# Kernel tuning notes

Hardware: AMD Instinct MI355X
Metric: run time of the kernel (lower is better)

## Reference

```python
import jax, jax.numpy as jnp
import numpy as np

# static config (matches init_kwargs / input_specs)
LENS = (2048, 1024, 512, 256)   # per-level temporal lengths, sum = 3840
N, LQ, D_MODEL = 8, 2048, 256
M, L, P = 8, 4, 4               # heads, levels, points
D_HEAD = D_MODEL // M           # 32


def setup_inputs() -> dict:
    key = jax.random.key(0)
    ks = jax.random.split(key, 8)
    s = 0.02  # xavier-ish scale for 256-wide linears
    return {
        "query": jax.random.normal(ks[0], (N, LQ, D_MODEL), jnp.float32),
        "reference_points": jax.random.uniform(ks[1], (N, LQ, L, 1), dtype=jnp.float32),
        "input_flatten": jax.random.normal(ks[2], (N, sum(LENS), D_MODEL), jnp.float32),
        "input_temporal_lens": jnp.array(LENS, jnp.int32),
        "input_level_start_index": jnp.array(np.concatenate([[0], np.cumsum(LENS)[:-1]]), jnp.int32),
        "W_val": jax.random.normal(ks[3], (D_MODEL, D_MODEL), jnp.float32) * s,
        "b_val": jnp.zeros((D_MODEL,), jnp.float32),
        "W_off": jax.random.normal(ks[4], (M * L * P, D_MODEL), jnp.float32) * s,
        "b_off": jax.random.normal(ks[5], (M * L * P,), jnp.float32),  # mimics linspace bias init
        "W_attn": jax.random.normal(ks[6], (M * L * P, D_MODEL), jnp.float32) * s,
        "b_attn": jnp.zeros((M * L * P,), jnp.float32),
    }


def _sample_level(v, x, T):
    """1D bilinear sampling with zero padding, matching F.grid_sample
    (mode='bilinear', padding_mode='zeros', align_corners=False) on a (1,T) map.
    v: (N, T, M, D) level values; x: (N, Lq, M, P) normalized locations in [0,1].
    Returns (N, Lq, M, P, D)."""
    n, lq, m, p = x.shape
    ix = x * T - 0.5
    ix0 = jnp.floor(ix)
    w1 = (ix - ix0)[..., None]            # (N,Lq,M,P,1)
    i0 = ix0.astype(jnp.int32)

    def gather(idx):
        valid = ((idx >= 0) & (idx < T)).astype(v.dtype)
        idxc = jnp.clip(idx, 0, T - 1)
        flat = idxc.transpose(0, 1, 3, 2).reshape(n, lq * p, m)       # (N, Lq*P, M)
        g = jnp.take_along_axis(v, flat[..., None], axis=1)           # (N, Lq*P, M, D)
        g = g * valid.transpose(0, 1, 3, 2).reshape(n, lq * p, m)[..., None]
        return g.reshape(n, lq, p, m, -1).transpose(0, 1, 3, 2, 4)    # (N,Lq,M,P,D)

    return gather(i0) * (1.0 - w1) + gather(i0 + 1) * w1


def _deform_core(value, lens, loc, attn):
    """value: (N, S, M, D); loc: (N,Lq,M,L,P,1); attn: (N,Lq,M,L,P) -> (N,Lq,M*D)"""
    out = 0.0
    start = 0
    for lid, T in enumerate(lens):
        v = value[:, start:start + T]
        start += T
        s = _sample_level(v, loc[:, :, :, lid, :, 0], T)              # (N,Lq,M,P,D)
        out = out + jnp.einsum('nqmpd,nqmp->nqmd', s, attn[:, :, :, lid])
    n, lq, m, d = out.shape
    return out.reshape(n, lq, m * d)


def reference(query, reference_points, input_flatten, input_temporal_lens,
              input_level_start_index, W_val, b_val, W_off, b_off, W_attn, b_attn):
    lens = LENS  # static per-level lengths (needed for static slicing)
    value = (input_flatten @ W_val.T + b_val).reshape(N, sum(lens), M, D_HEAD)
    offs = (query @ W_off.T + b_off).reshape(N, LQ, M, L, P, 1)
    attn = jax.nn.softmax((query @ W_attn.T + b_attn).reshape(N, LQ, M, L * P), axis=-1)
    attn = attn.reshape(N, LQ, M, L, P)
    # reference_points last dim == 1, offset_normalizer=None branch
    norm = jnp.asarray(lens, query.dtype)[None, None, None, :, None, None]
    loc = reference_points[:, :, None, :, None, :] + offs / norm      # (N,Lq,M,L,P,1)
    # fp32 path of the torch module returns the core output WITHOUT output_proj
    return _deform_core(value, lens, loc, attn)
```

## Files before the change

kernel.cpp:

```cpp
#include <hip/hip_runtime.h>
#include <hip/hip_bf16.h>
#include <cstddef>

namespace {

constexpr int NB    = 8;
constexpr int LQn   = 2048;
constexpr int DM    = 256;
constexpr int S_TOT = 3840;

typedef __attribute__((ext_vector_type(8))) short  short8;
typedef __attribute__((ext_vector_type(4))) float  f32x4;
typedef __attribute__((ext_vector_type(8))) _Float16 half8;
typedef __attribute__((ext_vector_type(4))) _Float16 half4;
typedef __attribute__((ext_vector_type(2))) _Float16 half2v;

union BF8 { __hip_bfloat162 h2[4]; short8 s8; };
__device__ inline short8 cvt8(const f32x4 a, const f32x4 b) {
  BF8 r;
  r.h2[0] = __float22bfloat162_rn(make_float2(a[0], a[1]));
  r.h2[1] = __float22bfloat162_rn(make_float2(a[2], a[3]));
  r.h2[2] = __float22bfloat162_rn(make_float2(b[0], b[1]));
  r.h2[3] = __float22bfloat162_rn(make_float2(b[2], b[3]));
  return r.s8;
}

union SMem {
  struct { short A[128 * 64]; short B[128 * 64]; } ab;
  _Float16 c[128 * 136];
};

__global__ __launch_bounds__(256) void gemm_bf16_k(
    const float* __restrict__ A_val, const float* __restrict__ A_prj,
    const float* __restrict__ W_val, const float* __restrict__ b_val,
    const float* __restrict__ W_off, const float* __restrict__ b_off,
    const float* __restrict__ W_att, const float* __restrict__ b_att,
    _Float16* __restrict__ out_val, _Float16* __restrict__ out_prj)
{
  __shared__ SMem sm;
  short* As = sm.ab.A;
  short* Bs = sm.ab.B;

  const int tid  = threadIdx.x;
  const int lane = tid & 63;
  const int wid  = tid >> 6;
  const int wm   = wid >> 1;
  const int wn   = wid & 1;

  const int id = blockIdx.x;
  const float *A, *W, *bias;
  _Float16* out;
  int r0, c0;
  if (id < 480) {
    const int rb = id >> 1, c = id & 1;
    A = A_val; out = out_val; r0 = rb * 128; c0 = c * 128;
    W = W_val + (size_t)c0 * DM; bias = b_val + c0;
  } else {
    const int j = id - 480, rb = j >> 1, c = j & 1;
    A = A_prj; out = out_prj; r0 = rb * 128; c0 = c * 128;
    W = c ? W_att : W_off; bias = c ? b_att : b_off;
  }

  f32x4 acc[4][4] = {};

  float bv[4];
  #pragma unroll
  for (int ni = 0; ni < 4; ++ni)
    bv[ni] = bias[wn * 64 + ni * 16 + (lane & 15)];

  f32x4 pa0[4], pa1[4], pw0[4], pw1[4];

  auto load_tiles = [&](int k0) {
    #pragma unroll
    for (int i = 0; i < 4; ++i) {
      const int ch  = tid + i * 256;
      const int row = ch >> 3;
      const int kg  = ch & 7;
      const size_t goff = (size_t)(r0 + row) * DM + k0 + kg * 8;
      pa0[i] = *reinterpret_cast<const f32x4*>(&A[goff]);
      pa1[i] = *reinterpret_cast<const f32x4*>(&A[goff + 4]);
      const size_t woff = (size_t)row * DM + k0 + kg * 8;
      pw0[i] = *reinterpret_cast<const f32x4*>(&W[woff]);
      pw1[i] = *reinterpret_cast<const f32x4*>(&W[woff + 4]);
    }
  };

  load_tiles(0);

  for (int k = 0; k < 4; ++k) {
    #pragma unroll
    for (int i = 0; i < 4; ++i) {
      const int ch  = tid + i * 256;
      const int row = ch >> 3;
      const int kg  = ch & 7;
      const short8 sa = cvt8(pa0[i], pa1[i]);
      const short8 sw = cvt8(pw0[i], pw1[i]);
      const int byte = row * 128 + ((kg * 16) ^ ((row & 7) << 4));
      *reinterpret_cast<short8*>(reinterpret_cast<char*>(As) + byte) = sa;
      *reinterpret_cast<short8*>(reinterpret_cast<char*>(Bs) + byte) = sw;
    }
    if (k < 3) load_tiles((k + 1) * 64);

    asm volatile("s_waitcnt lgkmcnt(0)" ::: "memory");
    __builtin_amdgcn_sched_barrier(0);
    __builtin_amdgcn_s_barrier();
    __builtin_amdgcn_sched_barrier(0);

    #pragma unroll
    for (int ks = 0; ks < 2; ++ks) {
      const int kb = (ks * 32 + (lane >> 4) * 8) * 2;
      short8 af[4], bf[4];
      #pragma unroll
      for (int mi = 0; mi < 4; ++mi) {
        const int row = wm * 64 + mi * 16 + (lane & 15);
        const int byte = row * 128 + (kb ^ ((row & 7) << 4));
        af[mi] = *reinterpret_cast<const short8*>(
            reinterpret_cast<const char*>(As) + byte);
      }
      #pragma unroll
      for (int ni = 0; ni < 4; ++ni) {
        const int col = wn * 64 + ni * 16 + (lane & 15);
        const int byte = col * 128 + (kb ^ ((col & 7) << 4));
        bf[ni] = *reinterpret_cast<const short8*>(
            reinterpret_cast<const char*>(Bs) + byte);
      }
      #pragma unroll
      for (int mi = 0; mi < 4; ++mi)
        #pragma unroll
        for (int ni = 0; ni < 4; ++ni)
          acc[mi][ni] = __builtin_amdgcn_mfma_f32_16x16x32_bf16(
              af[mi], bf[ni], acc[mi][ni], 0, 0, 0);
    }

    asm volatile("s_waitcnt lgkmcnt(0)" ::: "memory");
    __builtin_amdgcn_sched_barrier(0);
    __builtin_amdgcn_s_barrier();
    __builtin_amdgcn_sched_barrier(0);
  }

  #pragma unroll
  for (int mi = 0; mi < 4; ++mi) {
    const int row = wm * 64 + mi * 16 + (lane >> 4) * 4;
    #pragma unroll
    for (int ni = 0; ni < 4; ++ni) {
      const int col = wn * 64 + ni * 16 + (lane & 15);
      #pragma unroll
      for (int j = 0; j < 4; ++j)
        sm.c[(row + j) * 136 + col] = (_Float16)(acc[mi][ni][j] + bv[ni]);
    }
  }
  __syncthreads();
  #pragma unroll
  for (int i = 0; i < 8; ++i) {
    const int ch  = tid + i * 256;
    const int row = ch >> 4;
    const int cc  = ch & 15;
    const half8 v = *reinterpret_cast<const half8*>(&sm.c[row * 136 + cc * 8]);
    *reinterpret_cast<half8*>(&out[(size_t)(r0 + row) * DM + c0 + cc * 8]) = v;
  }
}

__global__ __launch_bounds__(512) void sample_k(
    const _Float16* __restrict__ proj,
    const float* __restrict__ refp,
    const _Float16* __restrict__ value,
    float* __restrict__ out)
{
  __shared__ uint4 tap_s[8][136];

  const int d     = blockIdx.x;
  const int n     = d & 7;
  const int chunk = d >> 3;
  const int row0q = n * LQn + chunk * 8;
  const int t     = threadIdx.x;

  const int lens[4]   = {2048, 1024, 512, 256};
  const int starts[4] = {0, 2048, 3072, 3584};

  if (t < 256) {
    const int q   = t >> 5;
    const int m   = (t >> 2) & 7;
    const int sub = t & 3;
    const int j0  = m * 16 + sub * 4;
    const size_t prow = (size_t)(row0q + q) * DM;

    const half4 offv = *reinterpret_cast<const half4*>(&proj[prow + j0]);
    const half4 lgv  = *reinterpret_cast<const half4*>(&proj[prow + 128 + j0]);
    float lg[4], off[4];
    #pragma unroll
    for (int i = 0; i < 4; ++i) { lg[i] = (float)lgv[i]; off[i] = (float)offv[i]; }

    float mx = fmaxf(fmaxf(lg[0], lg[1]), fmaxf(lg[2], lg[3]));
    mx = fmaxf(mx, __shfl_xor(mx, 1));
    mx = fmaxf(mx, __shfl_xor(mx, 2));
    float e[4], s = 0.f;
    #pragma unroll
    for (int i = 0; i < 4; ++i) { e[i] = __expf(lg[i] - mx); s += e[i]; }
    s += __shfl_xor(s, 1);
    s += __shfl_xor(s, 2);
    const float inv = 1.f / s;

    const int   T  = lens[sub];
    const int   st = starts[sub];
    const float fT = (float)T;
    const float rf = refp[(size_t)(row0q + q) * 4 + sub];
    #pragma unroll
    for (int i = 0; i < 4; ++i) {
      const float a  = e[i] * inv;
      const float ix = fmaf(rf, fT, off[i] - 0.5f);
      const float fl = floorf(ix);
      const float w1 = ix - fl;
      const int   i0 = (int)fl;
      const int   i1 = i0 + 1;
      const float wa = (i0 >= 0 && i0 < T) ? a * (1.f - w1) : 0.f;
      const float wb = (i1 >= 0 && i1 < T) ? a * w1 : 0.f;
      const int   r0b = (st + min(max(i0, 0), T - 1)) * 512;
      const int   r1b = (st + min(max(i1, 0), T - 1)) * 512;
      union { half2v h; unsigned u; } pw;
      pw.h.x = (_Float16)wa; pw.h.y = (_Float16)wb;
      uint4 ent; ent.x = pw.u; ent.y = (unsigned)r0b; ent.z = (unsigned)r1b; ent.w = 0u;
      tap_s[q][m * 17 + sub * 4 + i] = ent;
    }
  }
  __syncthreads();

  const int q  = t >> 6;
  const int l  = t & 63;
  const int m  = l >> 3;
  const int dg = l & 3;
  const int th = (l >> 2) & 1;
  const char* vb = reinterpret_cast<const char*>(value) +
                   (size_t)n * S_TOT * 512 + m * 64 + dg * 16;

  float acc[8] = {};
  #pragma unroll
  for (int i = 0; i < 8; ++i) {
    const uint4 e = tap_s[q][m * 17 + th * 8 + i];
    union { unsigned u; half2v h; } pw; pw.u = e.x;
    const float wa = (float)pw.h.x;
    const float wb = (float)pw.h.y;
    const half8 v0 = *reinterpret_cast<const half8*>(vb + e.y);
    const half8 v1 = *reinterpret_cast<const half8*>(vb + e.z);
    #pragma unroll
    for (int j = 0; j < 8; ++j)
      acc[j] = fmaf(wa, (float)v0[j], fmaf(wb, (float)v1[j], acc[j]));
  }

  #pragma unroll
  for (int j = 0; j < 8; ++j) acc[j] += __shfl_xor(acc[j], 4);

  if (th == 0) {
    float* op = &out[(size_t)(row0q + q) * DM + m * 32 + dg * 8];
    f32x4 o0 = {acc[0], acc[1], acc[2], acc[3]};
    f32x4 o1 = {acc[4], acc[5], acc[6], acc[7]};
    *reinterpret_cast<f32x4*>(op)     = o0;
    *reinterpret_cast<f32x4*>(op + 4) = o1;
  }
}

}

extern "C" void kernel_launch(void* const* d_in, const int* in_sizes, int n_in,
                              void* d_out, int out_size, void* d_ws, size_t ws_size,
                              hipStream_t stream) {
  const float* query  = (const float*)d_in[0];
  const float* refp   = (const float*)d_in[1];
  const float* inflat = (const float*)d_in[2];
  const float* W_val  = (const float*)d_in[5];
  const float* b_val  = (const float*)d_in[6];
  const float* W_off  = (const float*)d_in[7];
  const float* b_off  = (const float*)d_in[8];
  const float* W_attn = (const float*)d_in[9];
  const float* b_attn = (const float*)d_in[10];
  float* out = (float*)d_out;

  _Float16* value_h = (_Float16*)d_ws;
  _Float16* proj_h  = (_Float16*)((char*)d_ws +
                      (size_t)NB * S_TOT * DM * sizeof(_Float16));

  gemm_bf16_k<<<dim3(736), dim3(256), 0, stream>>>(
      inflat, query, W_val, b_val, W_off, b_off, W_attn, b_attn,
      value_h, proj_h);

  sample_k<<<dim3(NB * LQn / 8), dim3(512), 0, stream>>>(
      proj_h, refp, value_h, out);
}
```

Measured before the change: 42.99 us.

## Stop prefetching weight tiles, raise occupancy hint, and group blocks by row

```diff
diff --git a/kernel.cpp b/kernel.cpp
--- a/kernel.cpp
+++ b/kernel.cpp
@@ -30,7 +30,7 @@
   _Float16 c[128 * 136];
 };
 
-__global__ __launch_bounds__(256) void gemm_bf16_k(
+__global__ __launch_bounds__(256, 3) void gemm_bf16_k(
     const float* __restrict__ A_val, const float* __restrict__ A_prj,
     const float* __restrict__ W_val, const float* __restrict__ b_val,
     const float* __restrict__ W_off, const float* __restrict__ b_off,
@@ -52,11 +52,14 @@
   _Float16* out;
   int r0, c0;
   if (id < 480) {
-    const int rb = id >> 1, c = id & 1;
+    const int rb = (id >> 4) * 8 + (id & 7);
+    const int c  = (id >> 3) & 1;
     A = A_val; out = out_val; r0 = rb * 128; c0 = c * 128;
     W = W_val + (size_t)c0 * DM; bias = b_val + c0;
   } else {
-    const int j = id - 480, rb = j >> 1, c = j & 1;
+    const int j  = id - 480;
+    const int rb = (j >> 4) * 8 + (j & 7);
+    const int c  = (j >> 3) & 1;
     A = A_prj; out = out_prj; r0 = rb * 128; c0 = c * 128;
     W = c ? W_att : W_off; bias = c ? b_att : b_off;
   }
@@ -68,9 +71,9 @@
   for (int ni = 0; ni < 4; ++ni)
     bv[ni] = bias[wn * 64 + ni * 16 + (lane & 15)];
 
-  f32x4 pa0[4], pa1[4], pw0[4], pw1[4];
-
-  auto load_tiles = [&](int k0) {
+  f32x4 pa0[4], pa1[4];
+
+  auto load_A = [&](int k0) {
     #pragma unroll
     for (int i = 0; i < 4; ++i) {
       const int ch  = tid + i * 256;
@@ -79,27 +82,35 @@
       const size_t goff = (size_t)(r0 + row) * DM + k0 + kg * 8;
       pa0[i] = *reinterpret_cast<const f32x4*>(&A[goff]);
       pa1[i] = *reinterpret_cast<const f32x4*>(&A[goff + 4]);
+    }
+  };
+
+  load_A(0);
+
+  for (int k = 0; k < 4; ++k) {
+    const int k0 = k * 64;
+    #pragma unroll 2
+    for (int i = 0; i < 4; ++i) {
+      const int ch  = tid + i * 256;
+      const int row = ch >> 3;
+      const int kg  = ch & 7;
       const size_t woff = (size_t)row * DM + k0 + kg * 8;
-      pw0[i] = *reinterpret_cast<const f32x4*>(&W[woff]);
-      pw1[i] = *reinterpret_cast<const f32x4*>(&W[woff + 4]);
-    }
-  };
-
-  load_tiles(0);
-
-  for (int k = 0; k < 4; ++k) {
+      const f32x4 w0 = *reinterpret_cast<const f32x4*>(&W[woff]);
+      const f32x4 w1 = *reinterpret_cast<const f32x4*>(&W[woff + 4]);
+      const short8 sw = cvt8(w0, w1);
+      const int byte = row * 128 + ((kg * 16) ^ ((row & 7) << 4));
+      *reinterpret_cast<short8*>(reinterpret_cast<char*>(Bs) + byte) = sw;
+    }
     #pragma unroll
     for (int i = 0; i < 4; ++i) {
       const int ch  = tid + i * 256;
       const int row = ch >> 3;
       const int kg  = ch & 7;
       const short8 sa = cvt8(pa0[i], pa1[i]);
-      const short8 sw = cvt8(pw0[i], pw1[i]);
       const int byte = row * 128 + ((kg * 16) ^ ((row & 7) << 4));
       *reinterpret_cast<short8*>(reinterpret_cast<char*>(As) + byte) = sa;
-      *reinterpret_cast<short8*>(reinterpret_cast<char*>(Bs) + byte) = sw;
-    }
-    if (k < 3) load_tiles((k + 1) * 64);
+    }
+    if (k < 3) load_A(k0 + 64);
 
     asm volatile("s_waitcnt lgkmcnt(0)" ::: "memory");
     __builtin_amdgcn_sched_barrier(0);
```

New measurement: 41.85 us. 1.03x faster.
